# Kernel tuning notes

Hardware: AMD Instinct MI355X
Metric: run time of the kernel (lower is better)

## Reference

```python
import jax, jax.numpy as jnp
import numpy as np

B, S, H, GRID = 8, 4096, 1152, 64  # 64x64 patch grid, pooled 4x4 -> 256


def setup_inputs() -> dict:
    key = jax.random.key(0)
    k1, = jax.random.split(key, 1)
    hidden_states = jax.random.normal(k1, (B, S, H), dtype=jnp.float32)
    idx = jnp.arange(S, dtype=jnp.int32)
    pos = jnp.stack([idx % GRID, idx // GRID], axis=-1)  # (S,2) = (x,y)
    pixel_position_ids = jnp.broadcast_to(pos, (B, S, 2))
    padding_positions = jnp.zeros((B, S), dtype=bool)
    return {
        "hidden_states": hidden_states,
        "pixel_position_ids": pixel_position_ids,
        "padding_positions": padding_positions,
        "output_length": 256,
    }


def reference(hidden_states, pixel_position_ids, padding_positions, output_length):
    # 1) zero out padding rows
    hs = jnp.where(padding_positions[..., None], 0.0, hidden_states)
    hidden_size = hs.shape[-1]
    seq_len = hs.shape[1]
    k = int((seq_len // output_length) ** 0.5)
    k_sq = k * k
    assert k_sq * output_length == seq_len
    # 2) position-indexed 2D average pool via one-hot matmul
    clamped = jnp.clip(pixel_position_ids, 0).astype(jnp.int32)
    max_x = jnp.max(clamped[..., 0], axis=-1, keepdims=True) + 1  # [B,1]
    kern = clamped // k
    kernel_idxs = kern[..., 0] + (max_x // k) * kern[..., 1]  # [B,S]
    weights = jax.nn.one_hot(kernel_idxs, output_length, dtype=jnp.float32) / k_sq  # [B,S,L]
    pooled = jnp.einsum('bsl,bsh->blh', weights, hs.astype(jnp.float32)).astype(hs.dtype)
    pooler_mask = jnp.any(weights != 0, axis=1)  # [B,L]
    # 3) scale by sqrt(hidden_size)
    pooled = pooled * (hidden_size ** 0.5)
    return pooled, pooler_mask
```

## Files before the change

kernel.cpp:

```cpp
#include <hip/hip_runtime.h>
#include <math.h>

#define BB   8
#define SS   4096
#define HH   1152
#define LL   256
#define KP   4
#define KSQ  16
#define CAP  32
#define H4   (HH / 4)
#define TPB  256
#define TOK_PER_THR (SS / TPB)

__global__ __launch_bounds__(TPB) void fused_pool_kernel(
    const float* __restrict__ hs,
    const int* __restrict__ pos,
    const unsigned char* __restrict__ pad,
    float* __restrict__ out)
{
    const int bl = blockIdx.x;
    const int b  = bl >> 8;
    const int l  = bl & (LL - 1);
    const int t  = threadIdx.x;

    const int2* p = (const int2*)(pos + (size_t)b * SS * 2);
    const unsigned char* pb = pad + (size_t)b * SS;

    int2 v[TOK_PER_THR];
    int mx = 0;
#pragma unroll
    for (int i = 0; i < TOK_PER_THR; ++i) {
        v[i] = p[t + TPB * i];
        mx = max(mx, max(v[i].x, 0));
    }
#pragma unroll
    for (int off = 32; off >= 1; off >>= 1)
        mx = max(mx, __shfl_xor(mx, off));

    __shared__ int s_wmax[TPB / 64];
    __shared__ int s_cnt;
    __shared__ int s_list[CAP];
    if (t == 0) s_cnt = 0;
    if ((t & 63) == 0) s_wmax[t >> 6] = mx;
    __syncthreads();

    const int m = max(max(s_wmax[0], s_wmax[1]), max(s_wmax[2], s_wmax[3]));
    const int stride = (m + 1) / KP;

#pragma unroll
    for (int i = 0; i < TOK_PER_THR; ++i) {
        const int x = max(v[i].x, 0);
        const int y = max(v[i].y, 0);
        const int kidx = x / KP + stride * (y / KP);
        if (kidx == l) {
            const int s = t + TPB * i;
            const int slot = atomicAdd(&s_cnt, 1);
            if (slot < CAP)
                s_list[slot] = pb[s] ? -1 : s;
        }
    }
    __syncthreads();

    const int c  = s_cnt;
    const int cc = min(c, CAP);

    const float4* hb = (const float4*)hs + (size_t)b * SS * H4;

    float4 a0 = make_float4(0.f, 0.f, 0.f, 0.f);
    float4 a1 = make_float4(0.f, 0.f, 0.f, 0.f);
    const bool has2 = t < (H4 - TPB);

    for (int i = 0; i < cc; ++i) {
        const int s = s_list[i];
        if (s < 0) continue;
        const float4* row = hb + (size_t)s * H4;
        float4 v0 = row[t];
        a0.x += v0.x; a0.y += v0.y; a0.z += v0.z; a0.w += v0.w;
        if (has2) {
            float4 v1 = row[t + TPB];
            a1.x += v1.x; a1.y += v1.y; a1.z += v1.z; a1.w += v1.w;
        }
    }

    const float scale = sqrtf((float)HH) / (float)KSQ;
    a0.x *= scale; a0.y *= scale; a0.z *= scale; a0.w *= scale;
    a1.x *= scale; a1.y *= scale; a1.z *= scale; a1.w *= scale;

    float4* orow = (float4*)out + (size_t)bl * H4;
    orow[t] = a0;
    if (has2) orow[t + TPB] = a1;

    if (t == 0)
        out[(size_t)BB * LL * HH + bl] = (c > 0) ? 1.0f : 0.0f;
}

extern "C" void kernel_launch(void* const* d_in, const int* in_sizes, int n_in,
                              void* d_out, int out_size, void* d_ws, size_t ws_size,
                              hipStream_t stream) {
    const float* hs          = (const float*)d_in[0];
    const int*   pos         = (const int*)d_in[1];
    const unsigned char* pad = (const unsigned char*)d_in[2];

    fused_pool_kernel<<<BB * LL, TPB, 0, stream>>>(hs, pos, pad, (float*)d_out);
}
```

Baseline: 30.78 us.

## Process two output bins per block and use nontemporal loads/stores

Each block now handles two pooled bins, halving the number of blocks and amortizing the per-block scan of all 4096 position ids (now loaded as int4, two tokens per load). The gather loads and output stores use nontemporal builtins, a cache hint for streaming data. The trade-off is fewer blocks (1024) giving less parallelism, and the two bins are accumulated serially within a block.

Result: slower. 35.49 us (+15.3%).

```diff
diff --git a/kernel.cpp b/kernel.cpp
--- a/kernel.cpp
+++ b/kernel.cpp
@@ -10,7 +10,10 @@
 #define CAP  32
 #define H4   (HH / 4)
 #define TPB  256
-#define TOK_PER_THR (SS / TPB)
+#define NBIN 2
+#define I4_PER_THR (SS / (2 * TPB))
+
+typedef float f32x4 __attribute__((ext_vector_type(4)));
 
 __global__ __launch_bounds__(TPB) void fused_pool_kernel(
     const float* __restrict__ hs,
@@ -18,29 +21,29 @@
     const unsigned char* __restrict__ pad,
     float* __restrict__ out)
 {
-    const int bl = blockIdx.x;
-    const int b  = bl >> 8;
-    const int l  = bl & (LL - 1);
-    const int t  = threadIdx.x;
+    const int blk = blockIdx.x;
+    const int b   = blk >> 7;
+    const int l0  = (blk & 127) * NBIN;
+    const int t   = threadIdx.x;
 
-    const int2* p = (const int2*)(pos + (size_t)b * SS * 2);
+    const int4* p = (const int4*)(pos + (size_t)b * SS * 2);
     const unsigned char* pb = pad + (size_t)b * SS;
 
-    int2 v[TOK_PER_THR];
+    int4 v[I4_PER_THR];
     int mx = 0;
 #pragma unroll
-    for (int i = 0; i < TOK_PER_THR; ++i) {
+    for (int i = 0; i < I4_PER_THR; ++i) {
         v[i] = p[t + TPB * i];
-        mx = max(mx, max(v[i].x, 0));
+        mx = max(mx, max(max(v[i].x, v[i].z), 0));
     }
 #pragma unroll
     for (int off = 32; off >= 1; off >>= 1)
         mx = max(mx, __shfl_xor(mx, off));
 
     __shared__ int s_wmax[TPB / 64];
-    __shared__ int s_cnt;
-    __shared__ int s_list[CAP];
-    if (t == 0) s_cnt = 0;
+    __shared__ int s_cnt[NBIN];
+    __shared__ int s_list[NBIN][CAP];
+    if (t < NBIN) s_cnt[t] = 0;
     if ((t & 63) == 0) s_wmax[t >> 6] = mx;
     __syncthreads();
 
@@ -48,50 +51,63 @@
     const int stride = (m + 1) / KP;
 
 #pragma unroll
-    for (int i = 0; i < TOK_PER_THR; ++i) {
-        const int x = max(v[i].x, 0);
-        const int y = max(v[i].y, 0);
-        const int kidx = x / KP + stride * (y / KP);
-        if (kidx == l) {
-            const int s = t + TPB * i;
-            const int slot = atomicAdd(&s_cnt, 1);
-            if (slot < CAP)
-                s_list[slot] = pb[s] ? -1 : s;
+    for (int i = 0; i < I4_PER_THR; ++i) {
+        const int s0 = 2 * (t + TPB * i);
+        {
+            const int x = max(v[i].x, 0), y = max(v[i].y, 0);
+            const int kidx = x / KP + stride * (y / KP);
+            const int d = kidx - l0;
+            if (d == 0 || d == 1) {
+                const int slot = atomicAdd(&s_cnt[d], 1);
+                if (slot < CAP) s_list[d][slot] = pb[s0] ? -1 : s0;
+            }
+        }
+        {
+            const int x = max(v[i].z, 0), y = max(v[i].w, 0);
+            const int kidx = x / KP + stride * (y / KP);
+            const int d = kidx - l0;
+            if (d == 0 || d == 1) {
+                const int slot = atomicAdd(&s_cnt[d], 1);
+                if (slot < CAP) s_list[d][slot] = pb[s0 + 1] ? -1 : (s0 + 1);
+            }
         }
     }
     __syncthreads();
 
-    const int c  = s_cnt;
-    const int cc = min(c, CAP);
+    const f32x4* hb = (const f32x4*)hs + (size_t)b * SS * H4;
+    const bool has2 = t < (H4 - TPB);
+    const float scale = sqrtf((float)HH) / (float)KSQ;
 
-    const float4* hb = (const float4*)hs + (size_t)b * SS * H4;
+#pragma unroll
+    for (int j = 0; j < NBIN; ++j) {
+        const int c  = s_cnt[j];
+        const int cc = min(c, CAP);
 
-    float4 a0 = make_float4(0.f, 0.f, 0.f, 0.f);
-    float4 a1 = make_float4(0.f, 0.f, 0.f, 0.f);
-    const bool has2 = t < (H4 - TPB);
+        f32x4 a0 = {0.f, 0.f, 0.f, 0.f};
+        f32x4 a1 = {0.f, 0.f, 0.f, 0.f};
 
-    for (int i = 0; i < cc; ++i) {
-        const int s = s_list[i];
-        if (s < 0) continue;
-        const float4* row = hb + (size_t)s * H4;
-        float4 v0 = row[t];
-        a0.x += v0.x; a0.y += v0.y; a0.z += v0.z; a0.w += v0.w;
-        if (has2) {
-            float4 v1 = row[t + TPB];
-            a1.x += v1.x; a1.y += v1.y; a1.z += v1.z; a1.w += v1.w;
+        for (int i = 0; i < cc; ++i) {
+            const int s = s_list[j][i];
+            if (s < 0) continue;
+            const f32x4* row = hb + (size_t)s * H4;
+            f32x4 v0 = __builtin_nontemporal_load(row + t);
+            a0 += v0;
+            if (has2) {
+                f32x4 v1 = __builtin_nontemporal_load(row + t + TPB);
+                a1 += v1;
+            }
         }
+
+        a0 *= scale;
+        a1 *= scale;
+
+        f32x4* orow = (f32x4*)out + (size_t)(b * LL + l0 + j) * H4;
+        __builtin_nontemporal_store(a0, orow + t);
+        if (has2) __builtin_nontemporal_store(a1, orow + t + TPB);
+
+        if (t == 0)
+            out[(size_t)BB * LL * HH + b * LL + l0 + j] = (c > 0) ? 1.0f : 0.0f;
     }
-
-    const float scale = sqrtf((float)HH) / (float)KSQ;
-    a0.x *= scale; a0.y *= scale; a0.z *= scale; a0.w *= scale;
-    a1.x *= scale; a1.y *= scale; a1.z *= scale; a1.w *= scale;
-
-    float4* orow = (float4*)out + (size_t)bl * H4;
-    orow[t] = a0;
-    if (has2) orow[t + TPB] = a1;
-
-    if (t == 0)
-        out[(size_t)BB * LL * HH + bl] = (c > 0) ? 1.0f : 0.0f;
 }
 
 extern "C" void kernel_launch(void* const* d_in, const int* in_sizes, int n_in,
@@ -101,5 +117,6 @@
     const int*   pos         = (const int*)d_in[1];
     const unsigned char* pad = (const unsigned char*)d_in[2];
 
-    fused_pool_kernel<<<BB * LL, TPB, 0, stream>>>(hs, pos, pad, (float*)d_out);
+    fused_pool_kernel<<<BB * LL / NBIN, TPB, 0, stream>>>(hs, pos, pad,
+                                                          (float*)d_out);
 }
```

## Speculatively gather assumed grid rows while validating position ids, with fallback path

Applied to the files above, without the earlier changes.

The kernel now assumes the standard row-major 64x64 layout and loads the 16 hidden-state rows for its pooled cell at the same time as it reads the position ids. This overlaps the big row loads with the max/kidx computation instead of serializing them. Padding is handled with per-row weights read from shared memory. Each wavefront then checks that every token's computed kernel index matches the assumed layout, and falls back to the original list-gather path on any mismatch. The cost is extra work and duplicated reads when the layout differs from the assumption.

New measurement: 38.15 us. 1.24x slower.

```diff
diff --git a/kernel.cpp b/kernel.cpp
--- a/kernel.cpp
+++ b/kernel.cpp
@@ -10,7 +10,9 @@
 #define CAP  32
 #define H4   (HH / 4)
 #define TPB  256
-#define TOK_PER_THR (SS / TPB)
+#define I4   (SS / (2 * TPB))
+
+typedef float f32x4 __attribute__((ext_vector_type(4)));
 
 __global__ __launch_bounds__(TPB) void fused_pool_kernel(
     const float* __restrict__ hs,
@@ -23,73 +25,125 @@
     const int l  = bl & (LL - 1);
     const int t  = threadIdx.x;
 
-    const int2* p = (const int2*)(pos + (size_t)b * SS * 2);
+    const int x0 = (l & 15) * KP;
+    const int y0 = (l >> 4) * KP;
+
+    __shared__ float s_w[KSQ];
+    __shared__ int   s_wmax[TPB / 64];
+    __shared__ int   s_match;
+    __shared__ int   s_cnt;
+    __shared__ int   s_list[CAP];
+
     const unsigned char* pb = pad + (size_t)b * SS;
+    if (t < KSQ) {
+        const int sj = (y0 + (t >> 2)) * 64 + x0 + (t & 3);
+        s_w[t] = pb[sj] ? 0.f : 1.f;
+    }
+    if (t == 0) { s_match = 1; s_cnt = 0; }
+    __syncthreads();
 
-    int2 v[TOK_PER_THR];
-    int mx = 0;
+    const int4*  p4 = (const int4*)(pos + (size_t)b * SS * 2);
+    const f32x4* hb = (const f32x4*)hs + (size_t)b * SS * H4;
+    const bool has2 = t < (H4 - TPB);
+
+    int4 v[I4];
+    int  mx = 0;
+    f32x4 a0 = {0.f, 0.f, 0.f, 0.f};
+    f32x4 a1 = {0.f, 0.f, 0.f, 0.f};
+
 #pragma unroll
-    for (int i = 0; i < TOK_PER_THR; ++i) {
-        v[i] = p[t + TPB * i];
-        mx = max(mx, max(v[i].x, 0));
+    for (int i = 0; i < I4; ++i) {
+        v[i] = p4[t + TPB * i];
+        mx = max(mx, max(max(v[i].x, v[i].z), 0));
+#pragma unroll
+        for (int u = 0; u < 2; ++u) {
+            const int j  = 2 * i + u;
+            const int sj = (y0 + (j >> 2)) * 64 + x0 + (j & 3);
+            const f32x4* row = hb + (size_t)sj * H4;
+            const float w = s_w[j];
+            a0 += w * row[t];
+            if (has2) a1 += w * row[t + TPB];
+        }
     }
+
 #pragma unroll
     for (int off = 32; off >= 1; off >>= 1)
         mx = max(mx, __shfl_xor(mx, off));
-
-    __shared__ int s_wmax[TPB / 64];
-    __shared__ int s_cnt;
-    __shared__ int s_list[CAP];
-    if (t == 0) s_cnt = 0;
     if ((t & 63) == 0) s_wmax[t >> 6] = mx;
     __syncthreads();
-
     const int m = max(max(s_wmax[0], s_wmax[1]), max(s_wmax[2], s_wmax[3]));
     const int stride = (m + 1) / KP;
 
+    bool ok = true;
 #pragma unroll
-    for (int i = 0; i < TOK_PER_THR; ++i) {
-        const int x = max(v[i].x, 0);
-        const int y = max(v[i].y, 0);
-        const int kidx = x / KP + stride * (y / KP);
-        if (kidx == l) {
-            const int s = t + TPB * i;
-            const int slot = atomicAdd(&s_cnt, 1);
-            if (slot < CAP)
-                s_list[slot] = pb[s] ? -1 : s;
+    for (int i = 0; i < I4; ++i) {
+        const int s0 = 2 * (t + TPB * i);
+        {
+            const int x = max(v[i].x, 0), y = max(v[i].y, 0);
+            const int ki  = (x >> 2) + stride * (y >> 2);
+            const int ref = ((s0 & 63) >> 2) + 16 * (s0 >> 8);
+            ok = ok && (ki == ref);
+        }
+        {
+            const int s1 = s0 + 1;
+            const int x = max(v[i].z, 0), y = max(v[i].w, 0);
+            const int ki  = (x >> 2) + stride * (y >> 2);
+            const int ref = ((s1 & 63) >> 2) + 16 * (s1 >> 8);
+            ok = ok && (ki == ref);
+        }
+    }
+    if (!__all(ok) && (t & 63) == 0) atomicAnd(&s_match, 0);
+    __syncthreads();
+
+    const float scale = sqrtf((float)HH) / (float)KSQ;
+
+    if (s_match) {
+        a0 *= scale; a1 *= scale;
+        f32x4* orow = (f32x4*)out + (size_t)bl * H4;
+        orow[t] = a0;
+        if (has2) orow[t + TPB] = a1;
+        if (t == 0) out[(size_t)BB * LL * HH + bl] = 1.0f;
+        return;
+    }
+
+#pragma unroll
+    for (int i = 0; i < I4; ++i) {
+        const int s0 = 2 * (t + TPB * i);
+        {
+            const int x = max(v[i].x, 0), y = max(v[i].y, 0);
+            const int ki = (x >> 2) + stride * (y >> 2);
+            if (ki == l) {
+                const int slot = atomicAdd(&s_cnt, 1);
+                if (slot < CAP) s_list[slot] = pb[s0] ? -1 : s0;
+            }
+        }
+        {
+            const int s1 = s0 + 1;
+            const int x = max(v[i].z, 0), y = max(v[i].w, 0);
+            const int ki = (x >> 2) + stride * (y >> 2);
+            if (ki == l) {
+                const int slot = atomicAdd(&s_cnt, 1);
+                if (slot < CAP) s_list[slot] = pb[s1] ? -1 : (s1);
+            }
         }
     }
     __syncthreads();
 
     const int c  = s_cnt;
     const int cc = min(c, CAP);
-
-    const float4* hb = (const float4*)hs + (size_t)b * SS * H4;
-
-    float4 a0 = make_float4(0.f, 0.f, 0.f, 0.f);
-    float4 a1 = make_float4(0.f, 0.f, 0.f, 0.f);
-    const bool has2 = t < (H4 - TPB);
-
+    f32x4 b0 = {0.f, 0.f, 0.f, 0.f};
+    f32x4 b1 = {0.f, 0.f, 0.f, 0.f};
     for (int i = 0; i < cc; ++i) {
         const int s = s_list[i];
         if (s < 0) continue;
-        const float4* row = hb + (size_t)s * H4;
-        float4 v0 = row[t];
-        a0.x += v0.x; a0.y += v0.y; a0.z += v0.z; a0.w += v0.w;
-        if (has2) {
-            float4 v1 = row[t + TPB];
-            a1.x += v1.x; a1.y += v1.y; a1.z += v1.z; a1.w += v1.w;
-        }
+        const f32x4* row = hb + (size_t)s * H4;
+        b0 += row[t];
+        if (has2) b1 += row[t + TPB];
     }
-
-    const float scale = sqrtf((float)HH) / (float)KSQ;
-    a0.x *= scale; a0.y *= scale; a0.z *= scale; a0.w *= scale;
-    a1.x *= scale; a1.y *= scale; a1.z *= scale; a1.w *= scale;
-
-    float4* orow = (float4*)out + (size_t)bl * H4;
-    orow[t] = a0;
-    if (has2) orow[t + TPB] = a1;
-
+    b0 *= scale; b1 *= scale;
+    f32x4* orow = (f32x4*)out + (size_t)bl * H4;
+    orow[t] = b0;
+    if (has2) orow[t + TPB] = b1;
     if (t == 0)
         out[(size_t)BB * LL * HH + bl] = (c > 0) ? 1.0f : 0.0f;
 }
```
